# Performance work log

Hardware: AMD Instinct MI355X
Metric: run time of the kernel (lower is better)

Reference implementation:

```python
import jax, jax.numpy as jnp
import numpy as np

L = 4000      # num identities
C = 8         # num cameras; center bank is label-major: center j -> (label j//C, cam j%C)
T = 0.07      # temperature
HARD_NEG_K = 50
LAMDA = 0.5


def setup_inputs() -> dict:
    key = jax.random.key(0)
    k1, k2, k3, k4 = jax.random.split(key, 4)
    n, d = 256, 2048
    feats = jax.random.normal(k1, (n, d), dtype=jnp.float32)
    centers = jax.random.normal(k2, (L * C, d), dtype=jnp.float32)
    centers = centers / jnp.linalg.norm(centers, axis=1, keepdims=True)  # bank is kept unit-norm
    labels = jax.random.randint(k3, (n,), 0, L, dtype=jnp.int64)
    camids = jax.random.randint(k4, (n,), 0, C, dtype=jnp.int64)
    return {"feats": feats, "centers": centers, "labels": labels, "camids": camids, "epoch": 5}


def _cap_losses(feats, centers, labels, camids):
    n = feats.shape[0]
    M = centers.shape[0]
    feats = feats / jnp.linalg.norm(feats, axis=1, keepdims=True)  # F.normalize(p=2, dim=1)
    center_labels = jnp.arange(M) // C
    center_cams = jnp.arange(M) % C

    sims = jnp.einsum('nd,md->nm', feats, centers) / T  # [n, M] scaled similarities
    own_idx = labels * C + camids                        # cam_label_index[(label, cam)]
    own = sims[jnp.arange(n), own_idx]                   # numerator logits
    exp_sims = jnp.exp(sims)                             # unit vectors => sims <= 1/T ~ 14.3, safe

    # ---- intra-camera loss: denominator over centers sharing the sample's camid ----
    cam_mask = (center_cams[None, :] == camids[:, None])
    denom_intra = jnp.sum(exp_sims * cam_mask, axis=1)
    loss_i = own - jnp.log(denom_intra)                  # log(frac_up/frac_down)
    # mean per camid, then sum over camids present in the batch, negated
    ones = jnp.ones((n,), dtype=feats.dtype)
    cam_sums = jax.ops.segment_sum(loss_i, camids, num_segments=C)
    cam_cnts = jax.ops.segment_sum(ones, camids, num_segments=C)
    loss_intra = -jnp.sum(jnp.where(cam_cnts > 0, cam_sums / jnp.maximum(cam_cnts, 1.0), 0.0))

    # ---- inter loss: same-label centers + first-K hard negatives (in bank order) ----
    lbl_mask = (center_labels[None, :] == labels[:, None])
    other = ~lbl_mask
    # torch concatenates other-label centers in label order and takes the FIRST 50 (a slice,
    # not top-k); label-major bank order makes that = first 50 other-label centers by index.
    rank = jnp.cumsum(other.astype(jnp.int32), axis=1)
    hard_mask = other & (rank <= HARD_NEG_K)
    denom_inter = jnp.sum(exp_sims * lbl_mask, axis=1) + jnp.sum(exp_sims * hard_mask, axis=1)
    loss_j = own - jnp.log(denom_inter)
    lbl_sums = jax.ops.segment_sum(loss_j, labels, num_segments=L)
    lbl_cnts = jax.ops.segment_sum(ones, labels, num_segments=L)
    loss_inter = -jnp.sum(jnp.where(lbl_cnts > 0, lbl_sums / jnp.maximum(lbl_cnts, 1.0), 0.0))

    return loss_intra, loss_inter


def reference(feats, centers, labels, camids, epoch):
    loss_intra, loss_inter = _cap_losses(feats, centers, labels, camids)
    if epoch < 5:  # epoch is a static python int
        return loss_intra
    return jnp.stack([loss_intra, LAMDA * loss_inter])
```

## Files before the change

### kernel.cpp

```cpp
#include <hip/hip_runtime.h>

typedef __attribute__((ext_vector_type(8))) __bf16 bf16x8;
typedef __attribute__((ext_vector_type(4))) __bf16 bf16x4;
typedef __attribute__((ext_vector_type(4))) float f32x4;

#define N_SAMP 256
#define DIM    2048
#define NCENT  32000
#define INV_T  14.285714285714285714f
#define NWG    500

__global__ __launch_bounds__(256) void norm_kernel(const float* __restrict__ feats,
                                                   __bf16* __restrict__ fnorm) {
    int row = blockIdx.x;
    int tid = threadIdx.x;
    const float* src = feats + (size_t)row * DIM;
    float4 v0 = reinterpret_cast<const float4*>(src)[2 * tid];
    float4 v1 = reinterpret_cast<const float4*>(src)[2 * tid + 1];
    float ss = v0.x * v0.x + v0.y * v0.y + v0.z * v0.z + v0.w * v0.w
             + v1.x * v1.x + v1.y * v1.y + v1.z * v1.z + v1.w * v1.w;
    #pragma unroll
    for (int off = 1; off < 64; off <<= 1) ss += __shfl_xor(ss, off, 64);
    __shared__ float wsum[4];
    if ((tid & 63) == 0) wsum[tid >> 6] = ss;
    __syncthreads();
    float inv = 1.0f / sqrtf(wsum[0] + wsum[1] + wsum[2] + wsum[3]);
    bf16x8 o;
    o[0] = (__bf16)(v0.x * inv); o[1] = (__bf16)(v0.y * inv);
    o[2] = (__bf16)(v0.z * inv); o[3] = (__bf16)(v0.w * inv);
    o[4] = (__bf16)(v1.x * inv); o[5] = (__bf16)(v1.y * inv);
    o[6] = (__bf16)(v1.z * inv); o[7] = (__bf16)(v1.w * inv);
    *reinterpret_cast<bf16x8*>(fnorm + (size_t)row * DIM + tid * 8) = o;
}

__global__ __launch_bounds__(512, 2) void sims_kernel(
    const __bf16* __restrict__ fnorm, const float* __restrict__ centers,
    const int* __restrict__ labels, const int* __restrict__ camids,
    float* __restrict__ d_acc, float* __restrict__ d_own)
{
    __shared__ __align__(16) uint2 sA[2][1024];
    __shared__ __align__(16) uint2 sB[2][1024];

    const int tid  = threadIdx.x;
    const int wave = tid >> 6;
    const int lane = tid & 63;
    const int l15  = lane & 15;
    const int lhi  = lane >> 4;

    const int d   = blockIdx.x;
    const int xcd = d & 7, loc = d >> 3;
    const int lid = (xcd < 4 ? xcd * 63 : 252 + (xcd - 4) * 62) + loc;
    const int nb  = lid >> 1;
    const int mb  = lid & 1;

    const int wr = (wave >> 2) * 64;
    const int wc = (wave & 3) * 32;

    f32x4 acc[4][2] = {};

    float4 vB[2];
    uint4  vA;

    const float4* bsrc = reinterpret_cast<const float4*>(centers);
    const uint4*  asrc = reinterpret_cast<const uint4*>(fnorm);

    auto stage_load = [&](int step) {
        #pragma unroll
        for (int j = 0; j < 2; ++j) {
            int f = j * 512 + tid;
            int row = f >> 3, pos = f & 7;
            vB[j] = bsrc[(size_t)(nb * 128 + row) * 512 + step * 8 + pos];
        }
        {
            int row = tid >> 2, pos = tid & 3;
            vA = asrc[(size_t)(mb * 128 + row) * 256 + step * 4 + pos];
        }
    };
    auto stage_write = [&](int b) {
        #pragma unroll
        for (int j = 0; j < 2; ++j) {
            int f = j * 512 + tid;
            int row = f >> 3, pos = f & 7;
            int lin = row * 64 + pos * 8;
            int adr = lin ^ (((lin >> 7) & 7) << 4);
            bf16x4 o;
            o[0] = (__bf16)vB[j].x; o[1] = (__bf16)vB[j].y;
            o[2] = (__bf16)vB[j].z; o[3] = (__bf16)vB[j].w;
            sB[b][adr >> 3] = __builtin_bit_cast(uint2, o);
        }
        {
            int row = tid >> 2, pos = tid & 3;
            int lin = row * 64 + pos * 16;
            int adr = lin ^ (((lin >> 7) & 7) << 4);
            sA[b][adr >> 3]     = make_uint2(vA.x, vA.y);
            sA[b][(adr >> 3)+1] = make_uint2(vA.z, vA.w);
        }
    };
    auto compute = [&](int b) {
        bf16x8 af[4], bf[2];
        #pragma unroll
        for (int mi = 0; mi < 4; ++mi) {
            int lin = (wr + mi * 16 + l15) * 64 + lhi * 16;
            int adr = lin ^ (((lin >> 7) & 7) << 4);
            af[mi] = *reinterpret_cast<const bf16x8*>(&sA[b][adr >> 3]);
        }
        #pragma unroll
        for (int ni = 0; ni < 2; ++ni) {
            int lin = (wc + ni * 16 + l15) * 64 + lhi * 16;
            int adr = lin ^ (((lin >> 7) & 7) << 4);
            bf[ni] = *reinterpret_cast<const bf16x8*>(&sB[b][adr >> 3]);
        }
        #pragma unroll
        for (int mi = 0; mi < 4; ++mi)
            #pragma unroll
            for (int ni = 0; ni < 2; ++ni)
                acc[mi][ni] = __builtin_amdgcn_mfma_f32_16x16x32_bf16(
                    af[mi], bf[ni], acc[mi][ni], 0, 0, 0);
    };

    stage_load(0);
    stage_write(0);
    __syncthreads();
    int cur = 0;
    for (int step = 0; step < 64; ++step) {
        if (step < 63) stage_load(step + 1);
        compute(cur);
        if (step < 63) { stage_write(cur ^ 1); cur ^= 1; }
        __syncthreads();
    }

    float* slot = d_acc + (d & 7) * 512;
    #pragma unroll
    for (int mi = 0; mi < 4; ++mi) {
        #pragma unroll
        for (int r = 0; r < 4; ++r) {
            int i   = mb * 128 + wr + mi * 16 + lhi * 4 + r;
            int lab = labels[i], cam = camids[i];
            int oidx = lab * 8 + cam;
            float pi = 0.f, pj = 0.f;
            #pragma unroll
            for (int ni = 0; ni < 2; ++ni) {
                int c = nb * 128 + wc + ni * 16 + l15;
                float s = acc[mi][ni][r] * INV_T;
                float e = __expf(s);
                if ((l15 & 7) == cam) pi += e;
                bool ol = ((c >> 3) == lab);
                bool hard = (!ol) && (c < ((c < lab * 8) ? 50 : 58));
                if (ol || hard) pj += e;
                if (c == oidx) d_own[i] = s;
            }
            #pragma unroll
            for (int off = 1; off < 16; off <<= 1) {
                pi += __shfl_xor(pi, off, 64);
                pj += __shfl_xor(pj, off, 64);
            }
            if (l15 == 0) {
                atomicAdd(&slot[i], pi);
                atomicAdd(&slot[N_SAMP + i], pj);
            }
        }
    }
}

__global__ __launch_bounds__(256) void finalize_kernel(
    const float* __restrict__ d_acc, const float* __restrict__ d_own,
    const int* __restrict__ labels, const int* __restrict__ camids,
    float* __restrict__ out, int out_size)
{
    __shared__ int s_lab[N_SAMP], s_cam[N_SAMP];
    __shared__ float wsum[8];
    int tid = threadIdx.x;
    s_lab[tid] = labels[tid];
    s_cam[tid] = camids[tid];
    __syncthreads();
    int myl = s_lab[tid], myc = s_cam[tid];
    int nl = 0, nc = 0;
    for (int j = 0; j < N_SAMP; ++j) {
        nl += (s_lab[j] == myl);
        nc += (s_cam[j] == myc);
    }
    float di = 0.f, dj = 0.f;
    #pragma unroll
    for (int s = 0; s < 8; ++s) {
        di += d_acc[s * 512 + tid];
        dj += d_acc[s * 512 + 256 + tid];
    }
    float own = d_own[tid];
    float li = own - logf(di);
    float lj = own - logf(dj);
    float a = li / (float)nc;
    float b = lj / (float)nl;
    #pragma unroll
    for (int off = 1; off < 64; off <<= 1) {
        a += __shfl_xor(a, off, 64);
        b += __shfl_xor(b, off, 64);
    }
    if ((tid & 63) == 0) { wsum[tid >> 6] = a; wsum[4 + (tid >> 6)] = b; }
    __syncthreads();
    if (tid == 0) {
        float sa = wsum[0] + wsum[1] + wsum[2] + wsum[3];
        float sb = wsum[4] + wsum[5] + wsum[6] + wsum[7];
        out[0] = -sa;
        if (out_size > 1) out[1] = -0.5f * sb;
    }
}

extern "C" void kernel_launch(void* const* d_in, const int* in_sizes, int n_in,
                              void* d_out, int out_size, void* d_ws, size_t ws_size,
                              hipStream_t stream) {
    const float* feats   = (const float*)d_in[0];
    const float* centers = (const float*)d_in[1];
    const int*   labels  = (const int*)d_in[2];
    const int*   camids  = (const int*)d_in[3];
    float* out = (float*)d_out;

    __bf16* fnorm = (__bf16*)d_ws;
    float* d_acc  = (float*)((char*)d_ws + (size_t)N_SAMP * DIM * sizeof(__bf16));
    float* d_own  = d_acc + 8 * 2 * N_SAMP;

    hipMemsetAsync(d_acc, 0, 8 * 2 * N_SAMP * sizeof(float), stream);
    norm_kernel<<<N_SAMP, 256, 0, stream>>>(feats, fnorm);
    sims_kernel<<<NWG, 512, 0, stream>>>(fnorm, centers, labels, camids, d_acc, d_own);
    finalize_kernel<<<1, 256, 0, stream>>>(d_acc, d_own, labels, camids, out, out_size);
}
```

Before: 99.83 us.

## Deepen global-load prefetch, fold memset into norm kernel, raise occupancy hint

The main loop now keeps two register sets of global loads in flight, issuing the load for step t+2 while computing step t. Its barrier is a manual LDS waitcnt plus s_barrier rather than __syncthreads, which may let global loads stay outstanding across it. The accumulator memset is folded into the norm kernel to remove a separate launch. The launch-bounds occupancy hint rises from 2 to 4 waves per SIMD, which may force register spills given the added prefetch registers.

```diff
diff --git a/kernel.cpp b/kernel.cpp
--- a/kernel.cpp
+++ b/kernel.cpp
@@ -11,9 +11,11 @@
 #define NWG    500
 
 __global__ __launch_bounds__(256) void norm_kernel(const float* __restrict__ feats,
-                                                   __bf16* __restrict__ fnorm) {
+                                                   __bf16* __restrict__ fnorm,
+                                                   float* __restrict__ d_acc) {
     int row = blockIdx.x;
     int tid = threadIdx.x;
+    if (row < 16) d_acc[row * 256 + tid] = 0.f;
     const float* src = feats + (size_t)row * DIM;
     float4 v0 = reinterpret_cast<const float4*>(src)[2 * tid];
     float4 v1 = reinterpret_cast<const float4*>(src)[2 * tid + 1];
@@ -33,13 +35,13 @@
     *reinterpret_cast<bf16x8*>(fnorm + (size_t)row * DIM + tid * 8) = o;
 }
 
-__global__ __launch_bounds__(512, 2) void sims_kernel(
+__global__ __launch_bounds__(512, 4) void sims_kernel(
     const __bf16* __restrict__ fnorm, const float* __restrict__ centers,
     const int* __restrict__ labels, const int* __restrict__ camids,
     float* __restrict__ d_acc, float* __restrict__ d_own)
 {
-    __shared__ __align__(16) uint2 sA[2][1024];
-    __shared__ __align__(16) uint2 sB[2][1024];
+    __shared__ __align__(16) char sA[2][8192];
+    __shared__ __align__(16) char sB[2][8192];
 
     const int tid  = threadIdx.x;
     const int wave = tid >> 6;
@@ -58,57 +60,47 @@
 
     f32x4 acc[4][2] = {};
 
-    float4 vB[2];
-    uint4  vA;
-
     const float4* bsrc = reinterpret_cast<const float4*>(centers);
     const uint4*  asrc = reinterpret_cast<const uint4*>(fnorm);
 
-    auto stage_load = [&](int step) {
+    auto issue = [&](int step, float4& b0, float4& b1, uint4& a) {
+        int r0 = tid >> 3, p0 = tid & 7;
+        b0 = bsrc[(size_t)(nb * 128 + r0) * 512 + step * 8 + p0];
+        int r1 = (512 + tid) >> 3, p1 = tid & 7;
+        b1 = bsrc[(size_t)(nb * 128 + r1) * 512 + step * 8 + p1];
+        int ra = tid >> 2, pa = tid & 3;
+        a = asrc[(size_t)(mb * 128 + ra) * 256 + step * 4 + pa];
+    };
+    auto wrbuf = [&](int b, const float4& b0, const float4& b1, const uint4& a) {
         #pragma unroll
         for (int j = 0; j < 2; ++j) {
-            int f = j * 512 + tid;
-            int row = f >> 3, pos = f & 7;
-            vB[j] = bsrc[(size_t)(nb * 128 + row) * 512 + step * 8 + pos];
+            const float4& v = j ? b1 : b0;
+            int row = (j * 512 + tid) >> 3, pos = tid & 7;
+            int adr = (row * 64 + pos * 8) ^ ((row & 7) << 4);
+            bf16x4 o;
+            o[0] = (__bf16)v.x; o[1] = (__bf16)v.y;
+            o[2] = (__bf16)v.z; o[3] = (__bf16)v.w;
+            *reinterpret_cast<uint2*>(&sB[b][adr]) = __builtin_bit_cast(uint2, o);
         }
         {
             int row = tid >> 2, pos = tid & 3;
-            vA = asrc[(size_t)(mb * 128 + row) * 256 + step * 4 + pos];
-        }
-    };
-    auto stage_write = [&](int b) {
-        #pragma unroll
-        for (int j = 0; j < 2; ++j) {
-            int f = j * 512 + tid;
-            int row = f >> 3, pos = f & 7;
-            int lin = row * 64 + pos * 8;
-            int adr = lin ^ (((lin >> 7) & 7) << 4);
-            bf16x4 o;
-            o[0] = (__bf16)vB[j].x; o[1] = (__bf16)vB[j].y;
-            o[2] = (__bf16)vB[j].z; o[3] = (__bf16)vB[j].w;
-            sB[b][adr >> 3] = __builtin_bit_cast(uint2, o);
-        }
-        {
-            int row = tid >> 2, pos = tid & 3;
-            int lin = row * 64 + pos * 16;
-            int adr = lin ^ (((lin >> 7) & 7) << 4);
-            sA[b][adr >> 3]     = make_uint2(vA.x, vA.y);
-            sA[b][(adr >> 3)+1] = make_uint2(vA.z, vA.w);
+            int adr = (row * 64 + pos * 16) ^ ((row & 7) << 4);
+            *reinterpret_cast<uint4*>(&sA[b][adr]) = a;
         }
     };
     auto compute = [&](int b) {
         bf16x8 af[4], bf[2];
         #pragma unroll
         for (int mi = 0; mi < 4; ++mi) {
-            int lin = (wr + mi * 16 + l15) * 64 + lhi * 16;
-            int adr = lin ^ (((lin >> 7) & 7) << 4);
-            af[mi] = *reinterpret_cast<const bf16x8*>(&sA[b][adr >> 3]);
+            int row = wr + mi * 16 + l15;
+            int adr = (row * 64 + lhi * 16) ^ ((row & 7) << 4);
+            af[mi] = *reinterpret_cast<const bf16x8*>(&sA[b][adr]);
         }
         #pragma unroll
         for (int ni = 0; ni < 2; ++ni) {
-            int lin = (wc + ni * 16 + l15) * 64 + lhi * 16;
-            int adr = lin ^ (((lin >> 7) & 7) << 4);
-            bf[ni] = *reinterpret_cast<const bf16x8*>(&sB[b][adr >> 3]);
+            int row = wc + ni * 16 + l15;
+            int adr = (row * 64 + lhi * 16) ^ ((row & 7) << 4);
+            bf[ni] = *reinterpret_cast<const bf16x8*>(&sB[b][adr]);
         }
         #pragma unroll
         for (int mi = 0; mi < 4; ++mi)
@@ -117,16 +109,27 @@
                 acc[mi][ni] = __builtin_amdgcn_mfma_f32_16x16x32_bf16(
                     af[mi], bf[ni], acc[mi][ni], 0, 0, 0);
     };
-
-    stage_load(0);
-    stage_write(0);
-    __syncthreads();
-    int cur = 0;
-    for (int step = 0; step < 64; ++step) {
-        if (step < 63) stage_load(step + 1);
-        compute(cur);
-        if (step < 63) { stage_write(cur ^ 1); cur ^= 1; }
-        __syncthreads();
+    #define BAR() do { asm volatile("s_waitcnt lgkmcnt(0)" ::: "memory"); \
+                       __builtin_amdgcn_s_barrier(); } while (0)
+
+    float4 b0A, b1A; uint4 aA;
+    float4 b0B, b1B; uint4 aB;
+
+    issue(0, b0A, b1A, aA);
+    issue(1, b0B, b1B, aB);
+    wrbuf(0, b0A, b1A, aA);
+    BAR();
+    for (int t = 0; t < 64; t += 2) {
+        if (t + 2 < 64) issue(t + 2, b0A, b1A, aA);
+        compute(0);
+        wrbuf(1, b0B, b1B, aB);
+        BAR();
+        if (t + 3 < 64) issue(t + 3, b0B, b1B, aB);
+        compute(1);
+        if (t + 2 < 64) {
+            wrbuf(0, b0A, b1A, aA);
+            BAR();
+        }
     }
 
     float* slot = d_acc + (d & 7) * 512;
@@ -218,8 +221,7 @@
     float* d_acc  = (float*)((char*)d_ws + (size_t)N_SAMP * DIM * sizeof(__bf16));
     float* d_own  = d_acc + 8 * 2 * N_SAMP;
 
-    hipMemsetAsync(d_acc, 0, 8 * 2 * N_SAMP * sizeof(float), stream);
-    norm_kernel<<<N_SAMP, 256, 0, stream>>>(feats, fnorm);
+    norm_kernel<<<N_SAMP, 256, 0, stream>>>(feats, fnorm, d_acc);
     sims_kernel<<<NWG, 512, 0, stream>>>(fnorm, centers, labels, camids, d_acc, d_own);
     finalize_kernel<<<1, 256, 0, stream>>>(d_acc, d_own, labels, camids, out, out_size);
 }
```

Measured after the change: 89.61 us. -10.2%, faster.
